# Kernel optimization log

Measured on AMD Instinct MI355X. Metric: run time of the kernel, lower is better.

## Reference

```python
import jax, jax.numpy as jnp
import numpy as np

F_IN, F_OUT, H, L_ENC, L_DEC, HORIZON = 32, 8, 64, 2, 2, 48
B, T = 2048, 512


def _lstm_cell(x, h, c, Wih, Whh, bih, bhh):
    # PyTorch LSTMCell: gates ordered i, f, g, o
    g = x @ Wih.T + bih + h @ Whh.T + bhh
    i, f, gg, o = jnp.split(g, 4, axis=-1)
    c_new = jax.nn.sigmoid(f) * c + jax.nn.sigmoid(i) * jnp.tanh(gg)
    h_new = jax.nn.sigmoid(o) * jnp.tanh(c_new)
    return h_new, c_new


def setup_inputs() -> dict:
    key = jax.random.key(0)
    ks = jax.random.split(key, 16)
    s = 1.0 / np.sqrt(H)
    u = lambda k, shape: jax.random.uniform(k, shape, jnp.float32, -s, s)
    return {
        "X": jax.random.normal(ks[0], (B, T, F_IN), jnp.float32),
        "X_mask": jnp.ones((B, T, F_IN), jnp.float32),
        "W_emb": u(ks[1], (H, F_IN)),
        "b_emb": u(ks[2], (H,)),
        "enc_Wih": u(ks[3], (L_ENC, 4 * H, H)),
        "enc_Whh": u(ks[4], (L_ENC, 4 * H, H)),
        "enc_bih": u(ks[5], (L_ENC, 4 * H)),
        "enc_bhh": u(ks[6], (L_ENC, 4 * H)),
        "dec_Wih": u(ks[7], (L_DEC, 4 * H, H)),
        "dec_Whh": u(ks[8], (L_DEC, 4 * H, H)),
        "dec_bih": u(ks[9], (L_DEC, 4 * H)),
        "dec_bhh": u(ks[10], (L_DEC, 4 * H)),
        "W_reg": u(ks[11], (F_OUT, H)),
        "b_reg": u(ks[12], (F_OUT,)),
    }


def reference(X, X_mask, W_emb, b_emb, enc_Wih, enc_Whh, enc_bih, enc_bhh,
              dec_Wih, dec_Whh, dec_bih, dec_bhh, W_reg, b_reg):
    batch = X.shape[0]
    # Token embedding for all timesteps at once: [T, B, H]
    emb = jnp.einsum('btf,hf->tbh', X, W_emb) + b_emb

    h0 = jnp.zeros((L_ENC, batch, H), X.dtype)
    c0 = jnp.zeros((L_ENC, batch, H), X.dtype)

    def enc_step(carry, x_t):
        h, c = carry
        h_t = x_t
        hs, cs = [], []
        for i in range(L_ENC):
            h_t, c_t = _lstm_cell(h_t, h[i], c[i], enc_Wih[i], enc_Whh[i], enc_bih[i], enc_bhh[i])
            hs.append(h_t)
            cs.append(c_t)
        return (jnp.stack(hs), jnp.stack(cs)), None

    (h_enc, _), _ = jax.lax.scan(enc_step, (h0, c0), emb)

    # Decoder: hidden states initialized from encoder h, cells from zero
    c_dec0 = jnp.zeros((L_DEC, batch, H), X.dtype)

    def dec_step(carry, _):
        h, c = carry
        h_t = h[-1]
        hs, cs = [], []
        for i in range(L_DEC):
            h_t, c_t = _lstm_cell(h_t, h[i], c[i], dec_Wih[i], dec_Whh[i], dec_bih[i], dec_bhh[i])
            hs.append(h_t)
            cs.append(c_t)
        y_t = h_t @ W_reg.T + b_reg
        return (jnp.stack(hs), jnp.stack(cs)), y_t

    _, ys = jax.lax.scan(dec_step, (h_enc, c_dec0), None, length=HORIZON)
    return jnp.transpose(ys, (1, 0, 2))  # [B, horizon, F_OUT]
```

## Files before the change

kernel.cpp:

```cpp
#include <hip/hip_runtime.h>
#include <hip/hip_bf16.h>

typedef __bf16 bf16x8 __attribute__((ext_vector_type(8)));
typedef float  f32x4  __attribute__((ext_vector_type(4)));

#define MFMA16(a,b,c) __builtin_amdgcn_mfma_f32_16x16x32_bf16((a),(b),(c),0,0,0)

__device__ __forceinline__ bf16x8 cvt8(f32x4 a, f32x4 b){
  bf16x8 r;
  r[0]=(__bf16)a[0]; r[1]=(__bf16)a[1]; r[2]=(__bf16)a[2]; r[3]=(__bf16)a[3];
  r[4]=(__bf16)b[0]; r[5]=(__bf16)b[1]; r[6]=(__bf16)b[2]; r[7]=(__bf16)b[3];
  return r;
}
__device__ __forceinline__ bf16x8 ld8(const float* p){
  return cvt8(*(const f32x4*)p, *(const f32x4*)(p+4));
}
__device__ __forceinline__ float sigm(float x){
  return __builtin_amdgcn_rcpf(1.f + __expf(-x));
}
__device__ __forceinline__ float tanhx(float x){
  return 1.f - 2.f*__builtin_amdgcn_rcpf(1.f + __expf(2.f*x));
}
__device__ __forceinline__ f32x4 sp(float v){ return (f32x4){v,v,v,v}; }

extern "C" __global__ void __launch_bounds__(1024, 4)
seq2seq_kernel(const float* __restrict__ X,
               const float* __restrict__ Wemb, const float* __restrict__ bemb,
               const float* __restrict__ eWih, const float* __restrict__ eWhh,
               const float* __restrict__ ebih, const float* __restrict__ ebhh,
               const float* __restrict__ dWih, const float* __restrict__ dWhh,
               const float* __restrict__ dbih, const float* __restrict__ dbhh,
               const float* __restrict__ Wreg, const float* __restrict__ breg,
               float* __restrict__ out)
{
  __shared__ __align__(16) __bf16 XA[2][8][144];
  __shared__ __align__(16) __bf16 H1s[8][80];
  __shared__ __align__(16) float  Gm[2][8][264];

  const int tid  = (int)threadIdx.x;
  const int w    = tid >> 6;
  const int grp  = w >> 3;
  const bool g0  = (grp == 0);
  const int wt   = w & 7;
  const int lane = tid & 63;
  const int col  = lane & 15;
  const int quad = lane >> 4;
  const int row8 = col & 7;
  const int b0   = (int)blockIdx.x * 8;
  const int brow = b0 + row8;

  for (int i = tid; i < 2*8*144; i += 1024) (&XA[0][0][0])[i] = (__bf16)0.f;
  for (int i = tid; i < 8*80;    i += 1024) (&H1s[0][0])[i]   = (__bf16)0.f;

  bf16x8 wf[8];
  float  gb[2];
#pragma unroll
  for (int ti=0; ti<2; ++ti){
    const int n = 32*wt + 16*ti + col;
    gb[ti] = ebih[grp*256+n] + ebhh[grp*256+n];
#pragma unroll
    for (int ks=0; ks<4; ++ks){
      const float* srcw = (ks < 2) ? eWih : eWhh;
      wf[ti*4+ks] = ld8(srcw + ((size_t)(grp*256+n))*64 + (ks&1)*32 + quad*8);
    }
  }

  const int ue = (w&3)*16 + col;
  bf16x8 wembf;
  float eb = 0.f;
  const float* xb = X + (size_t)brow*512*32 + quad*8;
  f32x4 pa0, pb0, pa1, pb1;
  if (w < 4){
    wembf = ld8(Wemb + ue*32 + quad*8);
    eb = bemb[ue];
    pa1 = *(const f32x4*)(xb+32); pb1 = *(const f32x4*)(xb+36);
    pa0 = *(const f32x4*)(xb+64); pb0 = *(const f32x4*)(xb+68);
  }

  float cC = 0.f;

  auto GEMM0 = [&](const int I){
    const int Px = (I+1)&1, Pr = I&1;
    bf16x8 ax0 = *(const bf16x8*)&XA[Px][row8][ 0 + quad*8];
    bf16x8 ax1 = *(const bf16x8*)&XA[Px][row8][32 + quad*8];
    bf16x8 ah0 = *(const bf16x8*)&XA[Pr][row8][64 + quad*8];
    bf16x8 ah1 = *(const bf16x8*)&XA[Pr][row8][96 + quad*8];
    f32x4 A0 = sp(gb[0]), A1 = sp(gb[1]);
    A0=MFMA16(ax0,wf[0],A0); A1=MFMA16(ax0,wf[4],A1);
    A0=MFMA16(ax1,wf[1],A0); A1=MFMA16(ax1,wf[5],A1);
    A0=MFMA16(ah0,wf[2],A0); A1=MFMA16(ah0,wf[6],A1);
    A0=MFMA16(ah1,wf[3],A0); A1=MFMA16(ah1,wf[7],A1);
    if (I < 510 && w < 4){
      const int s = I&1;
      f32x4 xr0 = s ? pa1 : pa0, xr1 = s ? pb1 : pb0;
      f32x4 ea = MFMA16(cvt8(xr0,xr1), wembf, sp(eb));
      int tn = I+4; if (tn > 511) tn = 511;
      f32x4 na = *(const f32x4*)(xb + (size_t)tn*32);
      f32x4 nb = *(const f32x4*)(xb + (size_t)tn*32 + 4);
      if (s){ pa1=na; pb1=nb; } else { pa0=na; pb0=nb; }
      if (quad < 2){
#pragma unroll
        for (int r=0; r<4; ++r) XA[s][quad*4+r][ue] = (__bf16)ea[r];
      }
    }
    f32x4 t0 = (quad&2) ? A1 : A0;
    const int rb2 = (quad&1)*4;
    const int nn  = 32*wt + ((quad&2)?16:0) + col;
#pragma unroll
    for (int r=0; r<4; ++r) Gm[0][rb2+r][nn] = t0[r];
  };

  auto GEMM1 = [&](const int I){
    const int Pr = I&1;
    bf16x8 ah0 = *(const bf16x8*)&XA[Pr][row8][64 + quad*8];
    bf16x8 ah1 = *(const bf16x8*)&XA[Pr][row8][96 + quad*8];
    bf16x8 ag0 = *(const bf16x8*)&H1s[row8][quad*8];
    bf16x8 ag1 = *(const bf16x8*)&H1s[row8][32 + quad*8];
    f32x4 A0 = sp(gb[0]), A1 = sp(gb[1]);
    A0=MFMA16(ah0,wf[0],A0); A1=MFMA16(ah0,wf[4],A1);
    A0=MFMA16(ah1,wf[1],A0); A1=MFMA16(ah1,wf[5],A1);
    A0=MFMA16(ag0,wf[2],A0); A1=MFMA16(ag0,wf[6],A1);
    A0=MFMA16(ag1,wf[3],A0); A1=MFMA16(ag1,wf[7],A1);
    f32x4 t0 = (quad&2) ? A1 : A0;
    const int rb2 = (quad&1)*4;
    const int nn  = 32*wt + ((quad&2)?16:0) + col;
#pragma unroll
    for (int r=0; r<4; ++r) Gm[1][rb2+r][nn] = t0[r];
  };

  auto EW0 = [&](const int I){
    const int Pw = (I+1)&1;
    const float* g = Gm[0][wt];
    float i0=sigm(g[lane]),      f0=sigm(g[64+lane]);
    float gg=tanhx(g[128+lane]), o0=sigm(g[192+lane]);
    cC = f0*cC + i0*gg;
    XA[Pw][wt][64+lane] = (__bf16)(o0*tanhx(cC));
  };

  auto EW1 = [&](){
    const float* g = Gm[1][wt];
    float i1=sigm(g[lane]),      f1=sigm(g[64+lane]);
    float gg=tanhx(g[128+lane]), o1=sigm(g[192+lane]);
    cC = f1*cC + i1*gg;
    H1s[wt][lane] = (__bf16)(o1*tanhx(cC));
  };

  __syncthreads();

  if (w < 4){
    f32x4 x0a = *(const f32x4*)xb, x0b = *(const f32x4*)(xb+4);
    f32x4 e0 = MFMA16(cvt8(x0a,x0b), wembf, sp(eb));
    if (quad < 2){
#pragma unroll
      for (int r=0; r<4; ++r) XA[0][quad*4+r][ue] = (__bf16)e0[r];
    }
  }
  __syncthreads();
  if (g0) GEMM0(-1);
  __syncthreads();
  if (g0) EW0(-1);
  __syncthreads();

#define SLOT(I)                                              \
  if (g0) GEMM0(I); else { if ((I) > 0) EW1(); }             \
  __syncthreads();                                           \
  if (g0) EW0(I); else GEMM1(I);                             \
  __syncthreads();

  for (int ii=0; ii<255; ++ii){
    SLOT(2*ii)
    SLOT(2*ii+1)
  }
  SLOT(510)
#undef SLOT

  if (!g0) EW1();
  __syncthreads();
  if (!g0) GEMM1(511);
  __syncthreads();
  if (!g0) EW1();
  __syncthreads();

  for (int idx = tid; idx < 8*128; idx += 1024){
    int r = idx >> 7, cc = idx & 127;
    XA[0][r][cc] = (cc < 64) ? H1s[r][cc] : XA[1][r][cc];
  }
  bf16x8 wr0 = ld8(Wreg + (col&7)*64 +  0 + quad*8);
  bf16x8 wr1 = ld8(Wreg + (col&7)*64 + 32 + quad*8);
  const float rb = breg[col&7];
  float gbd[2];
#pragma unroll
  for (int l=0; l<2; ++l){
    const int n = 16*w + col;
    gbd[l] = dbih[l*256+n] + dbhh[l*256+n];
#pragma unroll
    for (int ks=0; ks<4; ++ks){
      const float* srcw = (ks < 2) ? dWih : dWhh;
      wf[l*4+ks] = ld8(srcw + ((size_t)(l*256+n))*64 + (ks&1)*32 + quad*8);
    }
  }
  cC = 0.f;
  __syncthreads();

  auto Ystore = [&](const int t){
    f32x4 ya = sp(rb);
    bf16x8 y0 = *(const bf16x8*)&H1s[row8][quad*8];
    bf16x8 y1 = *(const bf16x8*)&H1s[row8][32 + quad*8];
    ya = MFMA16(y0, wr0, ya);
    ya = MFMA16(y1, wr1, ya);
    if (quad < 2 && col < 8){
#pragma unroll
      for (int r=0; r<4; ++r)
        out[((size_t)(b0 + quad*4 + r)*48 + t)*8 + col] = ya[r];
    }
  };

  for (int t=0; t<48; ++t){
    {
      bf16x8 ax0 = *(const bf16x8*)&XA[0][row8][ 0 + quad*8];
      bf16x8 ax1 = *(const bf16x8*)&XA[0][row8][32 + quad*8];
      bf16x8 ah0 = *(const bf16x8*)&XA[0][row8][64 + quad*8];
      bf16x8 ah1 = *(const bf16x8*)&XA[0][row8][96 + quad*8];
      f32x4 B0 = sp(gbd[0]);
      B0=MFMA16(ax0,wf[0],B0);
      B0=MFMA16(ax1,wf[1],B0);
      B0=MFMA16(ah0,wf[2],B0);
      B0=MFMA16(ah1,wf[3],B0);
      if (quad < 2){
#pragma unroll
        for (int r=0; r<4; ++r) Gm[0][quad*4+r][16*w+col] = B0[r];
      }
      if (t && w == 0) Ystore(t-1);
    }
    __syncthreads();
    if (w < 8){
      const float* g = Gm[0][w];
      float i0=sigm(g[lane]),      f0=sigm(g[64+lane]);
      float gg=tanhx(g[128+lane]), o0=sigm(g[192+lane]);
      cC = f0*cC + i0*gg;
      XA[0][w][64+lane] = (__bf16)(o0*tanhx(cC));
    }
    __syncthreads();
    {
      bf16x8 ah0 = *(const bf16x8*)&XA[0][row8][64 + quad*8];
      bf16x8 ah1 = *(const bf16x8*)&XA[0][row8][96 + quad*8];
      bf16x8 ag0 = *(const bf16x8*)&H1s[row8][quad*8];
      bf16x8 ag1 = *(const bf16x8*)&H1s[row8][32 + quad*8];
      f32x4 B1 = sp(gbd[1]);
      B1=MFMA16(ah0,wf[4],B1);
      B1=MFMA16(ah1,wf[5],B1);
      B1=MFMA16(ag0,wf[6],B1);
      B1=MFMA16(ag1,wf[7],B1);
      if (quad < 2){
#pragma unroll
        for (int r=0; r<4; ++r) Gm[1][quad*4+r][16*w+col] = B1[r];
      }
    }
    __syncthreads();
    if (w >= 8){
      const int rw = w - 8;
      const float* g = Gm[1][rw];
      float i1=sigm(g[lane]),      f1=sigm(g[64+lane]);
      float gg=tanhx(g[128+lane]), o1=sigm(g[192+lane]);
      cC = f1*cC + i1*gg;
      __bf16 hb = (__bf16)(o1*tanhx(cC));
      H1s[rw][lane]   = hb;
      XA[0][rw][lane] = hb;
    }
    __syncthreads();
  }
  if (w == 0) Ystore(47);
}

extern "C" void kernel_launch(void* const* d_in, const int* in_sizes, int n_in,
                              void* d_out, int out_size, void* d_ws, size_t ws_size,
                              hipStream_t stream)
{
  (void)in_sizes; (void)n_in; (void)out_size; (void)d_ws; (void)ws_size;
  const float* X    = (const float*)d_in[0];
  const float* Wemb = (const float*)d_in[2];
  const float* bemb = (const float*)d_in[3];
  const float* eWih = (const float*)d_in[4];
  const float* eWhh = (const float*)d_in[5];
  const float* ebih = (const float*)d_in[6];
  const float* ebhh = (const float*)d_in[7];
  const float* dWih = (const float*)d_in[8];
  const float* dWhh = (const float*)d_in[9];
  const float* dbih = (const float*)d_in[10];
  const float* dbhh = (const float*)d_in[11];
  const float* Wreg = (const float*)d_in[12];
  const float* breg = (const float*)d_in[13];
  float* out = (float*)d_out;

  seq2seq_kernel<<<dim3(256), dim3(1024), 0, stream>>>(
      X, Wemb, bemb, eWih, eWhh, ebih, ebhh,
      dWih, dWhh, dbih, dbhh, Wreg, breg, out);
}
```

Measured before the change: 635.3 us.

## Fuse LSTM gate nonlinearities into MFMA epilogue via cross-lane DPP shuffles

The weight rows are permuted so that each wave's MFMA output tile holds all four gates (i,f,g,o) for a subset of hidden units. Lanes then exchange gate values through DPP row shifts and ds_swizzle instead of staging them through a shared-memory gate buffer. This removes the Gm LDS round trip and half of the per-timestep barriers in both the encoder and the decoder. Double-buffered H1s/XA keep the reads and writes race-free. The cost is extra lane-shuffle and select logic, and duplicated transcendental work in lanes whose results are discarded.

```diff
diff --git a/kernel.cpp b/kernel.cpp
--- a/kernel.cpp
+++ b/kernel.cpp
@@ -22,6 +22,14 @@
   return 1.f - 2.f*__builtin_amdgcn_rcpf(1.f + __expf(2.f*x));
 }
 __device__ __forceinline__ f32x4 sp(float v){ return (f32x4){v,v,v,v}; }
+
+__device__ __forceinline__ float dppx8(float v){
+  return __int_as_float(__builtin_amdgcn_update_dpp(
+      0, __float_as_int(v), 0x128, 0xF, 0xF, true));
+}
+__device__ __forceinline__ float swz4(float v){
+  return __int_as_float(__builtin_amdgcn_ds_swizzle(__float_as_int(v), 0x101F));
+}
 
 extern "C" __global__ void __launch_bounds__(1024, 4)
 seq2seq_kernel(const float* __restrict__ X,
@@ -33,9 +41,8 @@
                const float* __restrict__ Wreg, const float* __restrict__ breg,
                float* __restrict__ out)
 {
-  __shared__ __align__(16) __bf16 XA[2][8][144];
-  __shared__ __align__(16) __bf16 H1s[8][80];
-  __shared__ __align__(16) float  Gm[2][8][264];
+  __shared__ __align__(16) __bf16 XA[2][8][136];
+  __shared__ __align__(16) __bf16 H1s[2][8][72];
 
   const int tid  = (int)threadIdx.x;
   const int w    = tid >> 6;
@@ -49,14 +56,19 @@
   const int b0   = (int)blockIdx.x * 8;
   const int brow = b0 + row8;
 
-  for (int i = tid; i < 2*8*144; i += 1024) (&XA[0][0][0])[i] = (__bf16)0.f;
-  for (int i = tid; i < 8*80;    i += 1024) (&H1s[0][0])[i]   = (__bf16)0.f;
+  const bool hib = (col & 8) != 0;
+  const bool qhb = (quad & 2) != 0;
+  const int  ewr = 4*(quad & 1) + (hib ? 1 : 0) + (qhb ? 2 : 0);
+  const int  ewu = 8*wt + (col & 7);
+
+  for (int i = tid; i < 2*8*136; i += 1024) (&XA[0][0][0])[i]  = (__bf16)0.f;
+  for (int i = tid; i < 2*8*72;  i += 1024) (&H1s[0][0][0])[i] = (__bf16)0.f;
 
   bf16x8 wf[8];
   float  gb[2];
 #pragma unroll
   for (int ti=0; ti<2; ++ti){
-    const int n = 32*wt + 16*ti + col;
+    const int n = 64*(2*ti + (col>>3)) + 8*wt + (col&7);
     gb[ti] = ebih[grp*256+n] + ebhh[grp*256+n];
 #pragma unroll
     for (int ks=0; ks<4; ++ks){
@@ -79,7 +91,24 @@
 
   float cC = 0.f;
 
-  auto GEMM0 = [&](const int I){
+  auto EWF = [&](f32x4 A0, f32x4 A1, float& c) -> float {
+    float lo0 = qhb ? A0[2] : A0[0];
+    float hi0 = qhb ? A0[3] : A0[1];
+    float lo1 = qhb ? A1[2] : A1[0];
+    float hi1 = qhb ? A1[3] : A1[1];
+    float a0s = hib ? hi0 : lo0, a0x = hib ? lo0 : hi0;
+    float a1s = hib ? hi1 : lo1, a1x = hib ? lo1 : hi1;
+    float r0 = dppx8(a0x), r1 = dppx8(a1x);
+    float gi = hib ? r0  : a0s;
+    float gf = hib ? a0s : r0;
+    float gg = hib ? r1  : a1s;
+    float go = hib ? a1s : r1;
+    float i0 = sigm(gi), f0 = sigm(gf), gt = tanhx(gg), o0 = sigm(go);
+    c = f0*c + i0*gt;
+    return o0*tanhx(c);
+  };
+
+  auto FUSED0 = [&](const int I){
     const int Px = (I+1)&1, Pr = I&1;
     bf16x8 ax0 = *(const bf16x8*)&XA[Px][row8][ 0 + quad*8];
     bf16x8 ax1 = *(const bf16x8*)&XA[Px][row8][32 + quad*8];
@@ -103,46 +132,21 @@
         for (int r=0; r<4; ++r) XA[s][quad*4+r][ue] = (__bf16)ea[r];
       }
     }
-    f32x4 t0 = (quad&2) ? A1 : A0;
-    const int rb2 = (quad&1)*4;
-    const int nn  = 32*wt + ((quad&2)?16:0) + col;
-#pragma unroll
-    for (int r=0; r<4; ++r) Gm[0][rb2+r][nn] = t0[r];
-  };
-
-  auto GEMM1 = [&](const int I){
-    const int Pr = I&1;
+    XA[Px][ewr][64+ewu] = (__bf16)EWF(A0, A1, cC);
+  };
+
+  auto FUSED1 = [&](const int I){
+    const int Px = (I+1)&1, Pr = I&1;
     bf16x8 ah0 = *(const bf16x8*)&XA[Pr][row8][64 + quad*8];
     bf16x8 ah1 = *(const bf16x8*)&XA[Pr][row8][96 + quad*8];
-    bf16x8 ag0 = *(const bf16x8*)&H1s[row8][quad*8];
-    bf16x8 ag1 = *(const bf16x8*)&H1s[row8][32 + quad*8];
+    bf16x8 ag0 = *(const bf16x8*)&H1s[Px][row8][ 0 + quad*8];
+    bf16x8 ag1 = *(const bf16x8*)&H1s[Px][row8][32 + quad*8];
     f32x4 A0 = sp(gb[0]), A1 = sp(gb[1]);
     A0=MFMA16(ah0,wf[0],A0); A1=MFMA16(ah0,wf[4],A1);
     A0=MFMA16(ah1,wf[1],A0); A1=MFMA16(ah1,wf[5],A1);
     A0=MFMA16(ag0,wf[2],A0); A1=MFMA16(ag0,wf[6],A1);
     A0=MFMA16(ag1,wf[3],A0); A1=MFMA16(ag1,wf[7],A1);
-    f32x4 t0 = (quad&2) ? A1 : A0;
-    const int rb2 = (quad&1)*4;
-    const int nn  = 32*wt + ((quad&2)?16:0) + col;
-#pragma unroll
-    for (int r=0; r<4; ++r) Gm[1][rb2+r][nn] = t0[r];
-  };
-
-  auto EW0 = [&](const int I){
-    const int Pw = (I+1)&1;
-    const float* g = Gm[0][wt];
-    float i0=sigm(g[lane]),      f0=sigm(g[64+lane]);
-    float gg=tanhx(g[128+lane]), o0=sigm(g[192+lane]);
-    cC = f0*cC + i0*gg;
-    XA[Pw][wt][64+lane] = (__bf16)(o0*tanhx(cC));
-  };
-
-  auto EW1 = [&](){
-    const float* g = Gm[1][wt];
-    float i1=sigm(g[lane]),      f1=sigm(g[64+lane]);
-    float gg=tanhx(g[128+lane]), o1=sigm(g[192+lane]);
-    cC = f1*cC + i1*gg;
-    H1s[wt][lane] = (__bf16)(o1*tanhx(cC));
+    H1s[Pr][ewr][ewu] = (__bf16)EWF(A0, A1, cC);
   };
 
   __syncthreads();
@@ -156,17 +160,10 @@
     }
   }
   __syncthreads();
-  if (g0) GEMM0(-1);
-  __syncthreads();
-  if (g0) EW0(-1);
-  __syncthreads();
-
-#define SLOT(I)                                              \
-  if (g0) GEMM0(I); else { if ((I) > 0) EW1(); }             \
-  __syncthreads();                                           \
-  if (g0) EW0(I); else GEMM1(I);                             \
-  __syncthreads();
-
+  if (g0) FUSED0(-1);
+  __syncthreads();
+
+#define SLOT(I) { if (g0) FUSED0(I); else FUSED1(I); __syncthreads(); }
   for (int ii=0; ii<255; ++ii){
     SLOT(2*ii)
     SLOT(2*ii+1)
@@ -174,16 +171,11 @@
   SLOT(510)
 #undef SLOT
 
-  if (!g0) EW1();
-  __syncthreads();
-  if (!g0) GEMM1(511);
-  __syncthreads();
-  if (!g0) EW1();
-  __syncthreads();
-
-  for (int idx = tid; idx < 8*128; idx += 1024){
-    int r = idx >> 7, cc = idx & 127;
-    XA[0][r][cc] = (cc < 64) ? H1s[r][cc] : XA[1][r][cc];
+  if (!g0) FUSED1(511);
+  __syncthreads();
+
+  for (int idx = tid; idx < 8*64; idx += 1024){
+    XA[1][idx>>6][idx&63] = H1s[1][idx>>6][idx&63];
   }
   bf16x8 wr0 = ld8(Wreg + (col&7)*64 +  0 + quad*8);
   bf16x8 wr1 = ld8(Wreg + (col&7)*64 + 32 + quad*8);
@@ -191,7 +183,7 @@
   float gbd[2];
 #pragma unroll
   for (int l=0; l<2; ++l){
-    const int n = 16*w + col;
+    const int n = 64*(col>>2) + 4*w + (col&3);
     gbd[l] = dbih[l*256+n] + dbhh[l*256+n];
 #pragma unroll
     for (int ks=0; ks<4; ++ks){
@@ -199,13 +191,37 @@
       wf[l*4+ks] = ld8(srcw + ((size_t)(l*256+n))*64 + (ks&1)*32 + quad*8);
     }
   }
-  cC = 0.f;
-  __syncthreads();
+  const int  gated = col >> 2;
+  const bool b0d = (gated & 1) != 0;
+  const bool b1d = (gated & 2) != 0;
+  const int  rd  = 4*(quad & 1) + (b1d ? 1 : 0) + (qhb ? 2 : 0);
+  const int  udj = 4*w + (col & 3);
+  float cD0 = 0.f, cD1 = 0.f;
+  __syncthreads();
+
+  auto EWD = [&](f32x4 B, float& c) -> float {
+    float lo  = qhb ? B[2] : B[0];
+    float hi2 = qhb ? B[3] : B[1];
+    float a  = b1d ? hi2 : lo;
+    float ax = b1d ? lo  : hi2;
+    float pA = swz4(a);
+    float pB = swz4(ax);
+    float qA = dppx8(ax);
+    float qB = dppx8(pB);
+    float gi = b1d ? (b0d?qB:qA) : (b0d?pA:a);
+    float gf = b1d ? (b0d?qA:qB) : (b0d?a:pA);
+    float gg = b1d ? (b0d?pA:a) : (b0d?qB:qA);
+    float go = b1d ? (b0d?a:pA) : (b0d?qA:qB);
+    float i0 = sigm(gi), f0 = sigm(gf), gt = tanhx(gg), o0 = sigm(go);
+    c = f0*c + i0*gt;
+    return o0*tanhx(c);
+  };
 
   auto Ystore = [&](const int t){
+    const int hp = t&1;
     f32x4 ya = sp(rb);
-    bf16x8 y0 = *(const bf16x8*)&H1s[row8][quad*8];
-    bf16x8 y1 = *(const bf16x8*)&H1s[row8][32 + quad*8];
+    bf16x8 y0 = *(const bf16x8*)&H1s[hp][row8][ 0 + quad*8];
+    bf16x8 y1 = *(const bf16x8*)&H1s[hp][row8][32 + quad*8];
     ya = MFMA16(y0, wr0, ya);
     ya = MFMA16(y1, wr1, ya);
     if (quad < 2 && col < 8){
@@ -215,60 +231,40 @@
     }
   };
 
-  for (int t=0; t<48; ++t){
-    {
-      bf16x8 ax0 = *(const bf16x8*)&XA[0][row8][ 0 + quad*8];
-      bf16x8 ax1 = *(const bf16x8*)&XA[0][row8][32 + quad*8];
-      bf16x8 ah0 = *(const bf16x8*)&XA[0][row8][64 + quad*8];
-      bf16x8 ah1 = *(const bf16x8*)&XA[0][row8][96 + quad*8];
-      f32x4 B0 = sp(gbd[0]);
-      B0=MFMA16(ax0,wf[0],B0);
-      B0=MFMA16(ax1,wf[1],B0);
-      B0=MFMA16(ah0,wf[2],B0);
-      B0=MFMA16(ah1,wf[3],B0);
-      if (quad < 2){
-#pragma unroll
-        for (int r=0; r<4; ++r) Gm[0][quad*4+r][16*w+col] = B0[r];
-      }
-      if (t && w == 0) Ystore(t-1);
-    }
-    __syncthreads();
-    if (w < 8){
-      const float* g = Gm[0][w];
-      float i0=sigm(g[lane]),      f0=sigm(g[64+lane]);
-      float gg=tanhx(g[128+lane]), o0=sigm(g[192+lane]);
-      cC = f0*cC + i0*gg;
-      XA[0][w][64+lane] = (__bf16)(o0*tanhx(cC));
-    }
-    __syncthreads();
-    {
-      bf16x8 ah0 = *(const bf16x8*)&XA[0][row8][64 + quad*8];
-      bf16x8 ah1 = *(const bf16x8*)&XA[0][row8][96 + quad*8];
-      bf16x8 ag0 = *(const bf16x8*)&H1s[row8][quad*8];
-      bf16x8 ag1 = *(const bf16x8*)&H1s[row8][32 + quad*8];
-      f32x4 B1 = sp(gbd[1]);
-      B1=MFMA16(ah0,wf[4],B1);
-      B1=MFMA16(ah1,wf[5],B1);
-      B1=MFMA16(ag0,wf[6],B1);
-      B1=MFMA16(ag1,wf[7],B1);
-      if (quad < 2){
-#pragma unroll
-        for (int r=0; r<4; ++r) Gm[1][quad*4+r][16*w+col] = B1[r];
-      }
-    }
-    __syncthreads();
-    if (w >= 8){
-      const int rw = w - 8;
-      const float* g = Gm[1][rw];
-      float i1=sigm(g[lane]),      f1=sigm(g[64+lane]);
-      float gg=tanhx(g[128+lane]), o1=sigm(g[192+lane]);
-      cC = f1*cC + i1*gg;
-      __bf16 hb = (__bf16)(o1*tanhx(cC));
-      H1s[rw][lane]   = hb;
-      XA[0][rw][lane] = hb;
-    }
-    __syncthreads();
-  }
+#define DSTEP(T) {                                                         \
+    const int P = (T)&1, Pm = P^1;                                         \
+    {                                                                      \
+      bf16x8 ax0 = *(const bf16x8*)&XA[Pm][row8][ 0 + quad*8];             \
+      bf16x8 ax1 = *(const bf16x8*)&XA[Pm][row8][32 + quad*8];             \
+      bf16x8 ah0 = *(const bf16x8*)&XA[Pm][row8][64 + quad*8];             \
+      bf16x8 ah1 = *(const bf16x8*)&XA[Pm][row8][96 + quad*8];             \
+      f32x4 B0 = sp(gbd[0]);                                               \
+      B0=MFMA16(ax0,wf[0],B0); B0=MFMA16(ax1,wf[1],B0);                    \
+      B0=MFMA16(ah0,wf[2],B0); B0=MFMA16(ah1,wf[3],B0);                    \
+      float h = EWD(B0, cD0);                                              \
+      if (!b0d) XA[P][rd][64+udj] = (__bf16)h;                             \
+      if ((T) && w == 0) Ystore((T)-1);                                    \
+    }                                                                      \
+    __syncthreads();                                                       \
+    {                                                                      \
+      bf16x8 ah0 = *(const bf16x8*)&XA[P][row8][64 + quad*8];              \
+      bf16x8 ah1 = *(const bf16x8*)&XA[P][row8][96 + quad*8];              \
+      bf16x8 ag0 = *(const bf16x8*)&H1s[Pm][row8][ 0 + quad*8];            \
+      bf16x8 ag1 = *(const bf16x8*)&H1s[Pm][row8][32 + quad*8];            \
+      f32x4 B1 = sp(gbd[1]);                                               \
+      B1=MFMA16(ah0,wf[4],B1); B1=MFMA16(ah1,wf[5],B1);                    \
+      B1=MFMA16(ag0,wf[6],B1); B1=MFMA16(ag1,wf[7],B1);                    \
+      float h = EWD(B1, cD1);                                              \
+      if (!b0d){ H1s[P][rd][udj] = (__bf16)h; XA[P][rd][udj] = (__bf16)h; }\
+    }                                                                      \
+    __syncthreads();                                                       \
+  }
+
+  for (int tt=0; tt<24; ++tt){
+    DSTEP(2*tt)
+    DSTEP(2*tt+1)
+  }
+#undef DSTEP
   if (w == 0) Ystore(47);
 }
 
```

Result: faster. 607.8 us (-4.3%).
